# Optimization experiments

Hardware: AMD Instinct MI355X
Metric: run time of the kernel (lower is better)

Reference implementation:

```python
import jax, jax.numpy as jnp
import numpy as np

B, LD, LQ, H = 16, 1024, 512, 1024


def setup_inputs() -> dict:
    key = jax.random.key(0)
    k1, k2, k3, k4 = jax.random.split(key, 4)
    D = jax.random.normal(k1, (B, LD, H), dtype=jnp.float32)
    Q = jax.random.normal(k2, (B, LQ, H), dtype=jnp.float32)
    # Padding-style masks derived from random valid lengths (True = masked).
    doc_lens = jax.random.randint(k3, (B,), 1, LD + 1, dtype=jnp.int32)
    q_lens = jax.random.randint(k4, (B,), 1, LQ + 1, dtype=jnp.int32)
    doc_mask = (jnp.arange(LD)[None, None, :] >= doc_lens[:, None, None])  # [B,1,LD]
    query_mask = (jnp.arange(LQ)[None, None, :] >= q_lens[:, None, None])  # [B,1,LQ]
    return {"D": D, "Q": Q, "doc_mask": doc_mask, "query_mask": query_mask,
            "doc_lens": doc_lens}


def reference(D, Q, doc_mask, query_mask, doc_lens):
    # Bidirectional cross-attention scores
    A_d = jnp.einsum('bdh,bqh->bdq', D, Q)          # [B,LD,LQ]
    A_q = jnp.einsum('bqh,bdh->bqd', Q, D)          # [B,LQ,LD]
    A_d = jax.nn.softmax(jnp.where(query_mask, -jnp.inf, A_d), axis=-1)
    A_q = jax.nn.softmax(jnp.where(doc_mask, -jnp.inf, A_q), axis=-1)
    C_q = jnp.einsum('bqd,bdh->bqh', A_q, D)        # [B,LQ,H]
    query_output = jnp.concatenate([Q, C_q], axis=-1)   # [B,LQ,2H]
    C_D = jnp.einsum('bdq,bqh->bdh', A_d, query_output)  # [B,LD,2H]
    doc_output = jnp.concatenate([C_D, D], axis=-1)      # [B,LD,3H]
    # extract_last: gather row at index (doc_lens - 1) along the seq dim
    idx = (doc_lens - 1).astype(jnp.int32)[:, None, None]  # [B,1,1]
    last = jnp.take_along_axis(doc_output, jnp.broadcast_to(idx, (doc_output.shape[0], 1, doc_output.shape[-1])), axis=1)
    last = jnp.squeeze(last, axis=1)                      # [B,3H]
    return doc_output, query_output, last
```

## Files before the change

### kernel.cpp

```cpp
#include <hip/hip_runtime.h>

#define B_   16
#define LD_  1024
#define LQ_  512
#define H_   1024

#define OUT0_F 0ull
#define OUT1_F 50331648ull
#define OUT2_F 67108864ull

#define OFF_DH   0ull
#define OFF_DL   33554432ull
#define OFF_QH   67108864ull
#define OFF_QL   83886080ull
#define OFF_S    100663296ull
#define OFF_AD   134217728ull
#define OFF_AQ   150994944ull
#define OFF_DHT  167772160ull
#define OFF_QT   201326592ull
#define OFF_RM   234881024ull
#define OFF_RI   234946560ull
#define OFF_CM   235012096ull
#define OFF_CI   235044864ull
#define OFF_QLEN 235077632ull
#define OFF_RPM  235077888ull
#define OFF_RPS  235340032ull
#define OFF_CPM  235602176ull
#define OFF_CPS  235864320ull

typedef _Float16 half8 __attribute__((ext_vector_type(8)));
typedef _Float16 half4v __attribute__((ext_vector_type(4)));
typedef float floatx4 __attribute__((ext_vector_type(4)));

__device__ __forceinline__ void gll16(const _Float16* g, _Float16* l) {
#if __has_builtin(__builtin_amdgcn_global_load_lds)
  __builtin_amdgcn_global_load_lds(
      (const __attribute__((address_space(1))) unsigned int*)(unsigned long long)g,
      (__attribute__((address_space(3))) unsigned int*)(unsigned int)(unsigned long long)l,
      16, 0, 0);
#else
  int lane = threadIdx.x & 63;
  *(half8*)(l + lane * 8) = *(const half8*)(g + lane * 8);
#endif
}

__device__ __forceinline__ void omerge(float& m, float& s, float pm, float ps) {
  float nm = fmaxf(m, pm);
  s = s * __expf(m - nm) + ps * __expf(pm - nm);
  m = nm;
}

__global__ void k_qlens(const unsigned char* qm, int* qlens) {
  __shared__ unsigned or_hi, is_f32;
  __shared__ int scnt[B_];
  if (threadIdx.x == 0) { or_hi = 0u; is_f32 = 0u; }
  if (threadIdx.x < B_) scnt[threadIdx.x] = 0;
  __syncthreads();
  const unsigned* w = (const unsigned*)qm;
  unsigned lo = 0u, lf = 0u;
  for (int i = threadIdx.x; i < (B_ * LQ_) / 4; i += 256) {
    unsigned v = w[i];
    lo |= (v >> 8);
    if (v == 0x3F800000u) lf = 1u;
  }
  if (lo) atomicOr(&or_hi, 1u);
  if (lf) atomicOr(&is_f32, 1u);
  __syncthreads();
  int esize4 = (or_hi == 0u) || is_f32;
  for (int idx = threadIdx.x; idx < B_ * LQ_; idx += 256) {
    int b = idx >> 9;
    int z;
    if (esize4) z = (((const unsigned*)qm)[idx] == 0u);
    else        z = (qm[idx] == 0);
    if (z) atomicAdd(&scnt[b], 1);
  }
  __syncthreads();
  if (threadIdx.x < B_) qlens[threadIdx.x] = scnt[threadIdx.x];
}

__global__ __launch_bounds__(256) void k_cast(
    const float* __restrict__ Dp, const float* __restrict__ Qp,
    const int* __restrict__ dlens,
    _Float16* __restrict__ Dh, _Float16* __restrict__ Dl,
    _Float16* __restrict__ Qh, _Float16* __restrict__ Ql,
    _Float16* __restrict__ DhT, _Float16* __restrict__ QT,
    float* __restrict__ out) {
  __shared__ _Float16 T[64 * 66];
  int bid = blockIdx.x;
  int t = threadIdx.x;
  int r = t >> 2, cb = (t & 3) << 4;
  bool isD = bid < 4096;
  int b, r0, c0;
  const float* src;
  if (isD) {
    b = bid >> 8; int rest = bid & 255; r0 = (rest >> 4) << 6; c0 = (rest & 15) << 6;
    src = Dp + (size_t)b * LD_ * H_;
  } else {
    int t2 = bid - 4096;
    b = t2 >> 7; int rest = t2 & 127; r0 = (rest >> 4) << 6; c0 = (rest & 15) << 6;
    src = Qp + (size_t)b * LQ_ * H_;
  }
  size_t eoff = (size_t)(r0 + r) * H_ + c0 + cb;
  float4 v[4];
#pragma unroll
  for (int k = 0; k < 4; ++k) v[k] = *(const float4*)(src + eoff + (k << 2));
  half4v hi4[4], lo4[4];
#pragma unroll
  for (int k = 0; k < 4; ++k) {
    const float* f = (const float*)&v[k];
#pragma unroll
    for (int e = 0; e < 4; ++e) {
      _Float16 h = (_Float16)f[e];
      hi4[k][e] = h;
      lo4[k][e] = (_Float16)(f[e] - (float)h);
    }
  }
  if (isD) {
    _Float16* dh = Dh + (size_t)b * LD_ * H_ + eoff;
    _Float16* dl = Dl + (size_t)b * LD_ * H_ + eoff;
    float* dob = out + OUT0_F + (size_t)b * LD_ * 3072 + (size_t)(r0 + r) * 3072 + 2048 + c0 + cb;
#pragma unroll
    for (int k = 0; k < 4; ++k) {
      *(half4v*)(dh + (k << 2)) = hi4[k];
      *(half4v*)(dl + (k << 2)) = lo4[k];
      *(float4*)(dob + (k << 2)) = v[k];
    }
    if (r0 + r == dlens[b] - 1) {
      float* o2 = out + OUT2_F + (size_t)b * 3072 + 2048 + c0 + cb;
#pragma unroll
      for (int k = 0; k < 4; ++k) *(float4*)(o2 + (k << 2)) = v[k];
    }
  } else {
    _Float16* qh = Qh + (size_t)b * LQ_ * H_ + eoff;
    _Float16* ql = Ql + (size_t)b * LQ_ * H_ + eoff;
    float* qob = out + OUT1_F + (size_t)b * LQ_ * 2048 + (size_t)(r0 + r) * 2048 + c0 + cb;
#pragma unroll
    for (int k = 0; k < 4; ++k) {
      *(half4v*)(qh + (k << 2)) = hi4[k];
      *(half4v*)(ql + (k << 2)) = lo4[k];
      *(float4*)(qob + (k << 2)) = v[k];
    }
  }
#pragma unroll
  for (int k = 0; k < 4; ++k)
#pragma unroll
    for (int e = 0; e < 4; ++e)
      T[r * 66 + cb + (k << 2) + e] = hi4[k][e];
  __syncthreads();
  int ho = t >> 2, wb = (t & 3) << 4;
  half4v o[4];
#pragma unroll
  for (int k = 0; k < 4; ++k)
#pragma unroll
    for (int e = 0; e < 4; ++e)
      o[k][e] = T[(wb + (k << 2) + e) * 66 + ho];
  if (isD) {
    _Float16* dt = DhT + (size_t)b * H_ * LD_ + (size_t)(c0 + ho) * LD_ + r0 + wb;
#pragma unroll
    for (int k = 0; k < 4; ++k) *(half4v*)(dt + (k << 2)) = o[k];
  } else {
    _Float16* qt = QT + (size_t)b * 2048 * LQ_ + (size_t)(c0 + ho) * LQ_ + r0 + wb;
#pragma unroll
    for (int k = 0; k < 4; ++k) *(half4v*)(qt + (k << 2)) = o[k];
  }
}

__global__ __launch_bounds__(256) void k_gemm_scores(
    const _Float16* __restrict__ Dh, const _Float16* __restrict__ Dl,
    const _Float16* __restrict__ Qh, const _Float16* __restrict__ Ql,
    float* __restrict__ S, const int* __restrict__ qlens, const int* __restrict__ dlens,
    float* __restrict__ rowPM, float* __restrict__ rowPS,
    float* __restrict__ colPM, float* __restrict__ colPS) {
  int raw = blockIdx.x;
  int xcd = raw & 7, idx = raw >> 3;
  int b = xcd + ((idx >> 5) << 3);
  int t = idx & 31, tm = t >> 2, tn = t & 3;
  const int K = H_;
  const _Float16* Ah = Dh + (size_t)b * LD_ * H_;
  const _Float16* Al = Dl + (size_t)b * LD_ * H_;
  const _Float16* Bh = Qh + (size_t)b * LQ_ * H_;
  const _Float16* Bl = Ql + (size_t)b * LQ_ * H_;
  float* Cb = S + (size_t)b * LD_ * LQ_;

  __shared__ _Float16 sAh[128 * 32], sAl[128 * 32], sBh[128 * 32], sBl[128 * 32];
  int lane = threadIdx.x & 63, wave = threadIdx.x >> 6;
  int wm = wave >> 1, wn = wave & 1;
  int m0 = tm << 7, n0 = tn << 7;
  int srow = lane >> 2, scol = (lane & 3) << 3;

  floatx4 acc[4][4];
  floatx4 z = {0.f, 0.f, 0.f, 0.f};
#pragma unroll
  for (int i = 0; i < 4; ++i)
#pragma unroll
    for (int j = 0; j < 4; ++j) acc[i][j] = z;

  for (int k0 = 0; k0 < K; k0 += 32) {
#pragma unroll
    for (int ts = 0; ts < 2; ++ts) {
      int row = (wave << 5) + (ts << 4) + srow;
      int lo = ((wave << 5) + (ts << 4)) << 5;
      size_t ga = (size_t)(m0 + row) * K + k0 + scol;
      size_t gb = (size_t)(n0 + row) * K + k0 + scol;
      gll16(Ah + ga, sAh + lo);
      gll16(Al + ga, sAl + lo);
      gll16(Bh + gb, sBh + lo);
      gll16(Bl + gb, sBl + lo);
    }
    __syncthreads();
    int lk = (lane >> 4) << 3, lr = lane & 15;
    half8 ah[4], al4[4], bh[4], bl4[4];
#pragma unroll
    for (int i = 0; i < 4; ++i) {
      int ar = ((wm << 6) + (i << 4) + lr) << 5;
      int br = ((wn << 6) + (i << 4) + lr) << 5;
      ah[i]  = *(const half8*)(sAh + ar + lk);
      al4[i] = *(const half8*)(sAl + ar + lk);
      bh[i]  = *(const half8*)(sBh + br + lk);
      bl4[i] = *(const half8*)(sBl + br + lk);
    }
#pragma unroll
    for (int i = 0; i < 4; ++i)
#pragma unroll
      for (int j = 0; j < 4; ++j) {
        acc[i][j] = __builtin_amdgcn_mfma_f32_16x16x32_f16(ah[i],  bh[j],  acc[i][j], 0, 0, 0);
        acc[i][j] = __builtin_amdgcn_mfma_f32_16x16x32_f16(ah[i],  bl4[j], acc[i][j], 0, 0, 0);
        acc[i][j] = __builtin_amdgcn_mfma_f32_16x16x32_f16(al4[i], bh[j],  acc[i][j], 0, 0, 0);
      }
    __syncthreads();
  }
  int quad = lane >> 4, l15 = lane & 15;
#pragma unroll
  for (int i = 0; i < 4; ++i) {
    int mb = m0 + (wm << 6) + (i << 4) + (quad << 2);
#pragma unroll
    for (int j = 0; j < 4; ++j) {
      int n = n0 + (wn << 6) + (j << 4) + l15;
#pragma unroll
      for (int rr = 0; rr < 4; ++rr)
        Cb[(size_t)(mb + rr) * LQ_ + n] = acc[i][j][rr];
    }
  }
  int qlen = qlens[b], dlen = dlens[b];
  float* redM = (float*)sAh;
  float* redS = (float*)sAl;
  float* cdM  = (float*)sBh;
  float* cdS  = (float*)sBl;
#pragma unroll
  for (int i = 0; i < 4; ++i) {
#pragma unroll
    for (int rr = 0; rr < 4; ++rr) {
      float mx = -1e30f;
#pragma unroll
      for (int j = 0; j < 4; ++j) {
        int q = n0 + (wn << 6) + (j << 4) + l15;
        if (q < qlen) mx = fmaxf(mx, acc[i][j][rr]);
      }
      float s = 0.f;
#pragma unroll
      for (int j = 0; j < 4; ++j) {
        int q = n0 + (wn << 6) + (j << 4) + l15;
        if (q < qlen) s += __expf(acc[i][j][rr] - mx);
      }
#pragma unroll
      for (int off = 1; off < 16; off <<= 1) {
        float om = __shfl_xor(mx, off);
        float os = __shfl_xor(s, off);
        omerge(mx, s, om, os);
      }
      if (l15 == 0) {
        int rl = (wm << 6) + (i << 4) + (quad << 2) + rr;
        redM[(rl << 1) + wn] = mx;
        redS[(rl << 1) + wn] = s;
      }
    }
  }
#pragma unroll
  for (int j = 0; j < 4; ++j) {
    float mx = -1e30f;
#pragma unroll
    for (int i = 0; i < 4; ++i)
#pragma unroll
      for (int rr = 0; rr < 4; ++rr) {
        int d = m0 + (wm << 6) + (i << 4) + (quad << 2) + rr;
        if (d < dlen) mx = fmaxf(mx, acc[i][j][rr]);
      }
    float s = 0.f;
#pragma unroll
    for (int i = 0; i < 4; ++i)
#pragma unroll
      for (int rr = 0; rr < 4; ++rr) {
        int d = m0 + (wm << 6) + (i << 4) + (quad << 2) + rr;
        if (d < dlen) s += __expf(acc[i][j][rr] - mx);
      }
#pragma unroll
    for (int off = 16; off < 64; off <<= 1) {
      float om = __shfl_xor(mx, off);
      float os = __shfl_xor(s, off);
      omerge(mx, s, om, os);
    }
    if (quad == 0) {
      int cl = (wn << 6) + (j << 4) + l15;
      cdM[(cl << 1) + wm] = mx;
      cdS[(cl << 1) + wm] = s;
    }
  }
  __syncthreads();
  if (threadIdx.x < 128) {
    int rl = threadIdx.x;
    float m1 = redM[rl << 1], s1 = redS[rl << 1];
    omerge(m1, s1, redM[(rl << 1) + 1], redS[(rl << 1) + 1]);
    int gr = b * LD_ + m0 + rl;
    rowPM[tn * (B_ * LD_) + gr] = m1;
    rowPS[tn * (B_ * LD_) + gr] = s1;
  } else {
    int cl = threadIdx.x - 128;
    float m1 = cdM[cl << 1], s1 = cdS[cl << 1];
    omerge(m1, s1, cdM[(cl << 1) + 1], cdS[(cl << 1) + 1]);
    int gc = b * LQ_ + n0 + cl;
    colPM[tm * (B_ * LQ_) + gc] = m1;
    colPS[tm * (B_ * LQ_) + gc] = s1;
  }
}

__global__ void k_merge(const float* __restrict__ rowPM, const float* __restrict__ rowPS,
                        const float* __restrict__ colPM, const float* __restrict__ colPS,
                        float* rm, float* ri, float* cm2, float* ci) {
  int t = blockIdx.x * 256 + threadIdx.x;
  if (t < B_ * LD_) {
    float m = -1e30f, s = 0.f;
#pragma unroll
    for (int c = 0; c < 4; ++c) omerge(m, s, rowPM[c * (B_ * LD_) + t], rowPS[c * (B_ * LD_) + t]);
    rm[t] = m; ri[t] = 1.0f / s;
  } else if (t < B_ * LD_ + B_ * LQ_) {
    int u = t - B_ * LD_;
    float m = -1e30f, s = 0.f;
#pragma unroll
    for (int c = 0; c < 8; ++c) omerge(m, s, colPM[c * (B_ * LQ_) + u], colPS[c * (B_ * LQ_) + u]);
    cm2[u] = m; ci[u] = 1.0f / s;
  }
}

__global__ void k_normalize(const float* __restrict__ S,
                            const float* rowmax, const float* rowinv,
                            const float* colmax, const float* colinv,
                            const int* qlens, const int* dlens,
                            _Float16* __restrict__ Ad, _Float16* __restrict__ Aq) {
  int blk = blockIdx.x;
  int b = blk >> 7, rest = blk & 127, dt = rest >> 3, qt = rest & 7;
  int d0 = dt << 6, q0 = qt << 6;
  int c = threadIdx.x & 63, w = threadIdx.x >> 6;
  int qlen = qlens[b], dlen = dlens[b];
  __shared__ _Float16 T[64 * 66];
  const float* Sb = S + (size_t)b * LD_ * LQ_;
  int q = q0 + c;
  float cmq = colmax[(b << 9) + q], ciq = colinv[(b << 9) + q];
  for (int i = 0; i < 16; ++i) {
    int r = (i << 2) + w, d = d0 + r;
    float s = Sb[(size_t)d * LQ_ + q];
    float ad = (q < qlen) ? __expf(s - rowmax[(b << 10) + d]) * rowinv[(b << 10) + d] : 0.f;
    Ad[(size_t)b * LD_ * LQ_ + (size_t)d * LQ_ + q] = (_Float16)ad;
    float aq = (d < dlen) ? __expf(s - cmq) * ciq : 0.f;
    T[c * 66 + r] = (_Float16)aq;
  }
  __syncthreads();
  for (int i = 0; i < 16; ++i) {
    int rq = (i << 2) + w;
    Aq[(size_t)b * LQ_ * LD_ + (size_t)(q0 + rq) * LD_ + d0 + c] = T[rq * 66 + c];
  }
}

__global__ __launch_bounds__(256) void k_gemm_cq(const _Float16* __restrict__ Aq,
                                                 const _Float16* __restrict__ DhT,
                                                 _Float16* __restrict__ QT,
                                                 float* __restrict__ out) {
  int raw = blockIdx.x;
  int xcd = raw & 7, idx = raw >> 3;
  int b = xcd + ((idx >> 5) << 3);
  int t = idx & 31, tm = t >> 3, tn = t & 7;
  const int K = LD_;
  const _Float16* A = Aq + (size_t)b * LQ_ * LD_;
  const _Float16* Bm = DhT + (size_t)b * H_ * LD_;
  __shared__ _Float16 sA[128 * 32], sB[128 * 32];
  int lane = threadIdx.x & 63, wave = threadIdx.x >> 6;
  int wm = wave >> 1, wn = wave & 1;
  int m0 = tm << 7, n0 = tn << 7;
  int srow = lane >> 2, scol = (lane & 3) << 3;

  floatx4 acc[4][4];
  floatx4 z = {0.f, 0.f, 0.f, 0.f};
#pragma unroll
  for (int i = 0; i < 4; ++i)
#pragma unroll
    for (int j = 0; j < 4; ++j) acc[i][j] = z;

  for (int k0 = 0; k0 < K; k0 += 32) {
#pragma unroll
    for (int ts = 0; ts < 2; ++ts) {
      int row = (wave << 5) + (ts << 4) + srow;
      int lo = ((wave << 5) + (ts << 4)) << 5;
      gll16(A + (size_t)(m0 + row) * K + k0 + scol, sA + lo);
      gll16(Bm + (size_t)(n0 + row) * K + k0 + scol, sB + lo);
    }
    __syncthreads();
    int lk = (lane >> 4) << 3, lr = lane & 15;
    half8 af[4], bf[4];
#pragma unroll
    for (int i = 0; i < 4; ++i) {
      af[i] = *(const half8*)(sA + (((wm << 6) + (i << 4) + lr) << 5) + lk);
      bf[i] = *(const half8*)(sB + (((wn << 6) + (i << 4) + lr) << 5) + lk);
    }
#pragma unroll
    for (int i = 0; i < 4; ++i)
#pragma unroll
      for (int j = 0; j < 4; ++j)
        acc[i][j] = __builtin_amdgcn_mfma_f32_16x16x32_f16(af[i], bf[j], acc[i][j], 0, 0, 0);
    __syncthreads();
  }
  float* qoutb = out + OUT1_F + (size_t)b * LQ_ * 2048;
  _Float16* qtb = QT + (size_t)b * 2048 * LQ_;
  int quad = lane >> 4, l15 = lane & 15;
#pragma unroll
  for (int i = 0; i < 4; ++i) {
    int q = m0 + (wm << 6) + (i << 4) + (quad << 2);
#pragma unroll
    for (int j = 0; j < 4; ++j) {
      int h = n0 + (wn << 6) + (j << 4) + l15;
#pragma unroll
      for (int rr = 0; rr < 4; ++rr)
        qoutb[(size_t)(q + rr) * 2048 + 1024 + h] = acc[i][j][rr];
      half4v hv;
#pragma unroll
      for (int rr = 0; rr < 4; ++rr) hv[rr] = (_Float16)acc[i][j][rr];
      *(half4v*)(qtb + (size_t)(1024 + h) * LQ_ + q) = hv;
    }
  }
}

__global__ __launch_bounds__(256) void k_gemm_cd(const _Float16* __restrict__ Ad,
                                                 const _Float16* __restrict__ QT,
                                                 const int* __restrict__ dlens,
                                                 float* __restrict__ out) {
  int raw = blockIdx.x;
  int xcd = raw & 7, idx = raw >> 3;
  int b = xcd + ((idx >> 7) << 3);
  int tile = idx & 127, tm = tile >> 4, tn = tile & 15;
  const int K = LQ_;
  const _Float16* A = Ad + (size_t)b * LD_ * LQ_;
  const _Float16* Bm = QT + (size_t)b * 2048 * LQ_;
  __shared__ _Float16 sA[128 * 32], sB[128 * 32];
  int lane = threadIdx.x & 63, wave = threadIdx.x >> 6;
  int wm = wave >> 1, wn = wave & 1;
  int m0 = tm << 7, n0 = tn << 7;
  int srow = lane >> 2, scol = (lane & 3) << 3;

  floatx4 acc[4][4];
  floatx4 z = {0.f, 0.f, 0.f, 0.f};
#pragma unroll
  for (int i = 0; i < 4; ++i)
#pragma unroll
    for (int j = 0; j < 4; ++j) acc[i][j] = z;

  for (int k0 = 0; k0 < K; k0 += 32) {
#pragma unroll
    for (int ts = 0; ts < 2; ++ts) {
      int row = (wave << 5) + (ts << 4) + srow;
      int lo = ((wave << 5) + (ts << 4)) << 5;
      gll16(A + (size_t)(m0 + row) * K + k0 + scol, sA + lo);
      gll16(Bm + (size_t)(n0 + row) * K + k0 + scol, sB + lo);
    }
    __syncthreads();
    int lk = (lane >> 4) << 3, lr = lane & 15;
    half8 af[4], bf[4];
#pragma unroll
    for (int i = 0; i < 4; ++i) {
      af[i] = *(const half8*)(sA + (((wm << 6) + (i << 4) + lr) << 5) + lk);
      bf[i] = *(const half8*)(sB + (((wn << 6) + (i << 4) + lr) << 5) + lk);
    }
#pragma unroll
    for (int i = 0; i < 4; ++i)
#pragma unroll
      for (int j = 0; j < 4; ++j)
        acc[i][j] = __builtin_amdgcn_mfma_f32_16x16x32_f16(af[i], bf[j], acc[i][j], 0, 0, 0);
    __syncthreads();
  }
  float* db = out + OUT0_F + (size_t)b * LD_ * 3072;
  int dlast = dlens[b] - 1;
  int quad = lane >> 4, l15 = lane & 15;
#pragma unroll
  for (int i = 0; i < 4; ++i) {
    int mb = m0 + (wm << 6) + (i << 4) + (quad << 2);
#pragma unroll
    for (int j = 0; j < 4; ++j) {
      int n = n0 + (wn << 6) + (j << 4) + l15;
#pragma unroll
      for (int rr = 0; rr < 4; ++rr) {
        db[(size_t)(mb + rr) * 3072 + n] = acc[i][j][rr];
        if (mb + rr == dlast) out[OUT2_F + (size_t)b * 3072 + n] = acc[i][j][rr];
      }
    }
  }
}

extern "C" void kernel_launch(void* const* d_in, const int* in_sizes, int n_in,
                              void* d_out, int out_size, void* d_ws, size_t ws_size,
                              hipStream_t stream) {
  const float* Dp = (const float*)d_in[0];
  const float* Qp = (const float*)d_in[1];
  const unsigned char* qmask = (const unsigned char*)d_in[3];
  const int* dlens = (const int*)d_in[4];
  float* out = (float*)d_out;
  char* ws = (char*)d_ws;

  _Float16* Dh  = (_Float16*)(ws + OFF_DH);
  _Float16* Dl  = (_Float16*)(ws + OFF_DL);
  _Float16* Qh  = (_Float16*)(ws + OFF_QH);
  _Float16* Ql  = (_Float16*)(ws + OFF_QL);
  float*    S   = (float*)(ws + OFF_S);
  _Float16* Ad  = (_Float16*)(ws + OFF_AD);
  _Float16* Aq  = (_Float16*)(ws + OFF_AQ);
  _Float16* DhT = (_Float16*)(ws + OFF_DHT);
  _Float16* QT  = (_Float16*)(ws + OFF_QT);
  float*    rm  = (float*)(ws + OFF_RM);
  float*    ri  = (float*)(ws + OFF_RI);
  float*    cm  = (float*)(ws + OFF_CM);
  float*    ci  = (float*)(ws + OFF_CI);
  int*      ql  = (int*)(ws + OFF_QLEN);
  float*    rpm = (float*)(ws + OFF_RPM);
  float*    rps = (float*)(ws + OFF_RPS);
  float*    cpm = (float*)(ws + OFF_CPM);
  float*    cps = (float*)(ws + OFF_CPS);

  k_qlens<<<1, 256, 0, stream>>>(qmask, ql);
  k_cast<<<6144, 256, 0, stream>>>(Dp, Qp, dlens, Dh, Dl, Qh, Ql, DhT, QT, out);
  k_gemm_scores<<<512, 256, 0, stream>>>(Dh, Dl, Qh, Ql, S, ql, dlens, rpm, rps, cpm, cps);
  k_merge<<<96, 256, 0, stream>>>(rpm, rps, cpm, cps, rm, ri, cm, ci);
  k_normalize<<<2048, 256, 0, stream>>>(S, rm, ri, cm, ci, ql, dlens, Ad, Aq);
  k_gemm_cq<<<512, 256, 0, stream>>>(Aq, DhT, QT, out);
  k_gemm_cd<<<2048, 256, 0, stream>>>(Ad, QT, dlens, out);
}
```

Before: 585.2 us.

## Fuse qlen and merge kernels, vectorize normalize and transposed stores

```diff
diff --git a/kernel.cpp b/kernel.cpp
--- a/kernel.cpp
+++ b/kernel.cpp
@@ -18,10 +18,6 @@
 #define OFF_AQ   150994944ull
 #define OFF_DHT  167772160ull
 #define OFF_QT   201326592ull
-#define OFF_RM   234881024ull
-#define OFF_RI   234946560ull
-#define OFF_CM   235012096ull
-#define OFF_CI   235044864ull
 #define OFF_QLEN 235077632ull
 #define OFF_RPM  235077888ull
 #define OFF_RPS  235340032ull
@@ -50,43 +46,44 @@
   m = nm;
 }
 
-__global__ void k_qlens(const unsigned char* qm, int* qlens) {
-  __shared__ unsigned or_hi, is_f32;
-  __shared__ int scnt[B_];
-  if (threadIdx.x == 0) { or_hi = 0u; is_f32 = 0u; }
-  if (threadIdx.x < B_) scnt[threadIdx.x] = 0;
-  __syncthreads();
-  const unsigned* w = (const unsigned*)qm;
-  unsigned lo = 0u, lf = 0u;
-  for (int i = threadIdx.x; i < (B_ * LQ_) / 4; i += 256) {
-    unsigned v = w[i];
-    lo |= (v >> 8);
-    if (v == 0x3F800000u) lf = 1u;
-  }
-  if (lo) atomicOr(&or_hi, 1u);
-  if (lf) atomicOr(&is_f32, 1u);
-  __syncthreads();
-  int esize4 = (or_hi == 0u) || is_f32;
-  for (int idx = threadIdx.x; idx < B_ * LQ_; idx += 256) {
-    int b = idx >> 9;
-    int z;
-    if (esize4) z = (((const unsigned*)qm)[idx] == 0u);
-    else        z = (qm[idx] == 0);
-    if (z) atomicAdd(&scnt[b], 1);
-  }
-  __syncthreads();
-  if (threadIdx.x < B_) qlens[threadIdx.x] = scnt[threadIdx.x];
-}
-
 __global__ __launch_bounds__(256) void k_cast(
     const float* __restrict__ Dp, const float* __restrict__ Qp,
     const int* __restrict__ dlens,
+    const unsigned char* __restrict__ qm, int* __restrict__ qlens,
     _Float16* __restrict__ Dh, _Float16* __restrict__ Dl,
     _Float16* __restrict__ Qh, _Float16* __restrict__ Ql,
     _Float16* __restrict__ DhT, _Float16* __restrict__ QT,
     float* __restrict__ out) {
+  int bid = blockIdx.x;
+  if (bid == 6144) {
+    __shared__ unsigned or_hi, is_f32;
+    __shared__ int scnt[B_];
+    if (threadIdx.x == 0) { or_hi = 0u; is_f32 = 0u; }
+    if (threadIdx.x < B_) scnt[threadIdx.x] = 0;
+    __syncthreads();
+    const unsigned* w = (const unsigned*)qm;
+    unsigned lo = 0u, lf = 0u;
+    for (int i = threadIdx.x; i < (B_ * LQ_) / 4; i += 256) {
+      unsigned v = w[i];
+      lo |= (v >> 8);
+      if (v == 0x3F800000u) lf = 1u;
+    }
+    if (lo) atomicOr(&or_hi, 1u);
+    if (lf) atomicOr(&is_f32, 1u);
+    __syncthreads();
+    int esize4 = (or_hi == 0u) || is_f32;
+    for (int idx = threadIdx.x; idx < B_ * LQ_; idx += 256) {
+      int b = idx >> 9;
+      int z;
+      if (esize4) z = (((const unsigned*)qm)[idx] == 0u);
+      else        z = (qm[idx] == 0);
+      if (z) atomicAdd(&scnt[b], 1);
+    }
+    __syncthreads();
+    if (threadIdx.x < B_) qlens[threadIdx.x] = scnt[threadIdx.x];
+    return;
+  }
   __shared__ _Float16 T[64 * 66];
-  int bid = blockIdx.x;
   int t = threadIdx.x;
   int r = t >> 2, cb = (t & 3) << 4;
   bool isD = bid < 4096;
@@ -154,14 +151,20 @@
 #pragma unroll
     for (int e = 0; e < 4; ++e)
       o[k][e] = T[(wb + (k << 2) + e) * 66 + ho];
+  half8 h8a, h8b;
+#pragma unroll
+  for (int e = 0; e < 4; ++e) {
+    h8a[e] = o[0][e]; h8a[e + 4] = o[1][e];
+    h8b[e] = o[2][e]; h8b[e + 4] = o[3][e];
+  }
   if (isD) {
     _Float16* dt = DhT + (size_t)b * H_ * LD_ + (size_t)(c0 + ho) * LD_ + r0 + wb;
-#pragma unroll
-    for (int k = 0; k < 4; ++k) *(half4v*)(dt + (k << 2)) = o[k];
+    *(half8*)(dt) = h8a;
+    *(half8*)(dt + 8) = h8b;
   } else {
     _Float16* qt = QT + (size_t)b * 2048 * LQ_ + (size_t)(c0 + ho) * LQ_ + r0 + wb;
-#pragma unroll
-    for (int k = 0; k < 4; ++k) *(half4v*)(qt + (k << 2)) = o[k];
+    *(half8*)(qt) = h8a;
+    *(half8*)(qt + 8) = h8b;
   }
 }
 
@@ -323,50 +326,66 @@
   }
 }
 
-__global__ void k_merge(const float* __restrict__ rowPM, const float* __restrict__ rowPS,
-                        const float* __restrict__ colPM, const float* __restrict__ colPS,
-                        float* rm, float* ri, float* cm2, float* ci) {
-  int t = blockIdx.x * 256 + threadIdx.x;
-  if (t < B_ * LD_) {
-    float m = -1e30f, s = 0.f;
-#pragma unroll
-    for (int c = 0; c < 4; ++c) omerge(m, s, rowPM[c * (B_ * LD_) + t], rowPS[c * (B_ * LD_) + t]);
-    rm[t] = m; ri[t] = 1.0f / s;
-  } else if (t < B_ * LD_ + B_ * LQ_) {
-    int u = t - B_ * LD_;
-    float m = -1e30f, s = 0.f;
-#pragma unroll
-    for (int c = 0; c < 8; ++c) omerge(m, s, colPM[c * (B_ * LQ_) + u], colPS[c * (B_ * LQ_) + u]);
-    cm2[u] = m; ci[u] = 1.0f / s;
-  }
-}
-
-__global__ void k_normalize(const float* __restrict__ S,
-                            const float* rowmax, const float* rowinv,
-                            const float* colmax, const float* colinv,
-                            const int* qlens, const int* dlens,
-                            _Float16* __restrict__ Ad, _Float16* __restrict__ Aq) {
+__global__ __launch_bounds__(256) void k_normalize(
+    const float* __restrict__ S,
+    const float* __restrict__ rowPM, const float* __restrict__ rowPS,
+    const float* __restrict__ colPM, const float* __restrict__ colPS,
+    const int* __restrict__ qlens, const int* __restrict__ dlens,
+    _Float16* __restrict__ Ad, _Float16* __restrict__ Aq) {
   int blk = blockIdx.x;
   int b = blk >> 7, rest = blk & 127, dt = rest >> 3, qt = rest & 7;
   int d0 = dt << 6, q0 = qt << 6;
-  int c = threadIdx.x & 63, w = threadIdx.x >> 6;
+  int t = threadIdx.x;
+  __shared__ float sRM[64], sRI[64], sCM[64], sCI[64];
+  __shared__ _Float16 T[64 * 66];
+  if (t < 64) {
+    int gr = (b << 10) + d0 + t;
+    float m = -1e30f, s = 0.f;
+#pragma unroll
+    for (int c = 0; c < 4; ++c) omerge(m, s, rowPM[c * (B_ * LD_) + gr], rowPS[c * (B_ * LD_) + gr]);
+    sRM[t] = m; sRI[t] = 1.0f / s;
+  } else if (t < 128) {
+    int u = t - 64;
+    int gc = (b << 9) + q0 + u;
+    float m = -1e30f, s = 0.f;
+#pragma unroll
+    for (int c = 0; c < 8; ++c) omerge(m, s, colPM[c * (B_ * LQ_) + gc], colPS[c * (B_ * LQ_) + gc]);
+    sCM[u] = m; sCI[u] = 1.0f / s;
+  }
+  __syncthreads();
   int qlen = qlens[b], dlen = dlens[b];
-  __shared__ _Float16 T[64 * 66];
   const float* Sb = S + (size_t)b * LD_ * LQ_;
-  int q = q0 + c;
-  float cmq = colmax[(b << 9) + q], ciq = colinv[(b << 9) + q];
-  for (int i = 0; i < 16; ++i) {
-    int r = (i << 2) + w, d = d0 + r;
-    float s = Sb[(size_t)d * LQ_ + q];
-    float ad = (q < qlen) ? __expf(s - rowmax[(b << 10) + d]) * rowinv[(b << 10) + d] : 0.f;
-    Ad[(size_t)b * LD_ * LQ_ + (size_t)d * LQ_ + q] = (_Float16)ad;
-    float aq = (d < dlen) ? __expf(s - cmq) * ciq : 0.f;
-    T[c * 66 + r] = (_Float16)aq;
+  int qq = t & 15, dr = t >> 4;
+  float cm4[4], ci4[4];
+#pragma unroll
+  for (int e = 0; e < 4; ++e) { cm4[e] = sCM[(qq << 2) + e]; ci4[e] = sCI[(qq << 2) + e]; }
+#pragma unroll
+  for (int it = 0; it < 4; ++it) {
+    int dl_ = (it << 4) + dr, d = d0 + dl_;
+    float4 s4 = *(const float4*)(Sb + (size_t)d * LQ_ + q0 + (qq << 2));
+    float rm = sRM[dl_], ri = sRI[dl_];
+    const float* sv = (const float*)&s4;
+    bool dvalid = d < dlen;
+    half4v adv;
+#pragma unroll
+    for (int e = 0; e < 4; ++e) {
+      int q = q0 + (qq << 2) + e;
+      float ad = (q < qlen) ? __expf(sv[e] - rm) * ri : 0.f;
+      adv[e] = (_Float16)ad;
+      float aq = dvalid ? __expf(sv[e] - cm4[e]) * ci4[e] : 0.f;
+      T[((qq << 2) + e) * 66 + dl_] = (_Float16)aq;
+    }
+    *(half4v*)(Ad + (size_t)b * LD_ * LQ_ + (size_t)d * LQ_ + q0 + (qq << 2)) = adv;
   }
   __syncthreads();
-  for (int i = 0; i < 16; ++i) {
-    int rq = (i << 2) + w;
-    Aq[(size_t)b * LQ_ * LD_ + (size_t)(q0 + rq) * LD_ + d0 + c] = T[rq * 66 + c];
+  int c4 = (t & 15) << 2, rq0 = t >> 4;
+#pragma unroll
+  for (int it = 0; it < 4; ++it) {
+    int row = (it << 4) + rq0;
+    half4v v;
+#pragma unroll
+    for (int e = 0; e < 4; ++e) v[e] = T[row * 66 + c4 + e];
+    *(half4v*)(Aq + (size_t)b * LQ_ * LD_ + (size_t)(q0 + row) * LD_ + d0 + c4) = v;
   }
 }
 
@@ -381,7 +400,9 @@
   const int K = LD_;
   const _Float16* A = Aq + (size_t)b * LQ_ * LD_;
   const _Float16* Bm = DhT + (size_t)b * H_ * LD_;
-  __shared__ _Float16 sA[128 * 32], sB[128 * 32];
+  __shared__ _Float16 smem[64 * 136];
+  _Float16* sA = smem;
+  _Float16* sB = smem + 128 * 32;
   int lane = threadIdx.x & 63, wave = threadIdx.x >> 6;
   int wm = wave >> 1, wn = wave & 1;
   int m0 = tm << 7, n0 = tn << 7;
@@ -429,11 +450,32 @@
 #pragma unroll
       for (int rr = 0; rr < 4; ++rr)
         qoutb[(size_t)(q + rr) * 2048 + 1024 + h] = acc[i][j][rr];
-      half4v hv;
-#pragma unroll
-      for (int rr = 0; rr < 4; ++rr) hv[rr] = (_Float16)acc[i][j][rr];
-      *(half4v*)(qtb + (size_t)(1024 + h) * LQ_ + q) = hv;
-    }
+    }
+  }
+  _Float16* sT = smem;
+#pragma unroll 1
+  for (int p = 0; p < 2; ++p) {
+    __syncthreads();
+    if (wn == p) {
+#pragma unroll
+      for (int i = 0; i < 4; ++i) {
+        int ql_ = (wm << 6) + (i << 4) + (quad << 2);
+#pragma unroll
+        for (int j = 0; j < 4; ++j) {
+          int hl = (j << 4) + l15;
+#pragma unroll
+          for (int rr = 0; rr < 4; ++rr)
+            sT[hl * 136 + ql_ + rr] = (_Float16)acc[i][j][rr];
+        }
+      }
+    }
+    __syncthreads();
+    int row = threadIdx.x >> 2, ch = (threadIdx.x & 3) << 5;
+    _Float16* dst = qtb + (size_t)(1024 + n0 + (p << 6) + row) * LQ_ + m0 + ch;
+    const _Float16* srcp = sT + row * 136 + ch;
+#pragma unroll
+    for (int k = 0; k < 4; ++k)
+      *(half8*)(dst + (k << 3)) = *(const half8*)(srcp + (k << 3));
   }
 }
 
@@ -521,21 +563,15 @@
   _Float16* Aq  = (_Float16*)(ws + OFF_AQ);
   _Float16* DhT = (_Float16*)(ws + OFF_DHT);
   _Float16* QT  = (_Float16*)(ws + OFF_QT);
-  float*    rm  = (float*)(ws + OFF_RM);
-  float*    ri  = (float*)(ws + OFF_RI);
-  float*    cm  = (float*)(ws + OFF_CM);
-  float*    ci  = (float*)(ws + OFF_CI);
   int*      ql  = (int*)(ws + OFF_QLEN);
   float*    rpm = (float*)(ws + OFF_RPM);
   float*    rps = (float*)(ws + OFF_RPS);
   float*    cpm = (float*)(ws + OFF_CPM);
   float*    cps = (float*)(ws + OFF_CPS);
 
-  k_qlens<<<1, 256, 0, stream>>>(qmask, ql);
-  k_cast<<<6144, 256, 0, stream>>>(Dp, Qp, dlens, Dh, Dl, Qh, Ql, DhT, QT, out);
+  k_cast<<<6145, 256, 0, stream>>>(Dp, Qp, dlens, qmask, ql, Dh, Dl, Qh, Ql, DhT, QT, out);
   k_gemm_scores<<<512, 256, 0, stream>>>(Dh, Dl, Qh, Ql, S, ql, dlens, rpm, rps, cpm, cps);
-  k_merge<<<96, 256, 0, stream>>>(rpm, rps, cpm, cps, rm, ri, cm, ci);
-  k_normalize<<<2048, 256, 0, stream>>>(S, rm, ri, cm, ci, ql, dlens, Ad, Aq);
+  k_normalize<<<2048, 256, 0, stream>>>(S, rpm, rps, cpm, cps, ql, dlens, Ad, Aq);
   k_gemm_cq<<<512, 256, 0, stream>>>(Aq, DhT, QT, out);
   k_gemm_cd<<<2048, 256, 0, stream>>>(Ad, QT, dlens, out);
 }
```

Measured after the change: 571.5 us. -2.3%, faster.
